# Performance work log

Measured on AMD Instinct MI355X. Metric: run time of the kernel, lower is better.

Reference implementation:

```python
import jax, jax.numpy as jnp
import numpy as np

HEADS = 4
OUT_DIM = 32
NUM_NODES = 10000
NUM_EDGES = 640000  # avg degree 64


def setup_inputs() -> dict:
    key = jax.random.key(0)
    k1, k2, k3, k4 = jax.random.split(key, 4)
    HE = HEADS * NUM_EDGES
    x_i = jax.random.normal(k1, (HE, OUT_DIM), dtype=jnp.float32)
    x_j = jax.random.normal(k2, (HE, OUT_DIM), dtype=jnp.float32)
    # glorot init for a: [heads, 1, 2*out_dim]
    fan = 1 + 2 * OUT_DIM
    limit = np.sqrt(6.0 / fan)
    a = jax.random.uniform(k3, (HEADS, 1, 2 * OUT_DIM), dtype=jnp.float32,
                           minval=-limit, maxval=limit)
    # edge_index[1] holds per-head-offset destination node ids in [0, heads*num_nodes)
    edge_index = jax.random.randint(k4, (2, HE), 0, HEADS * NUM_NODES, dtype=jnp.int64)
    return {"x_i": x_i, "x_j": x_j, "a": a, "edge_index": edge_index,
            "num_nodes": NUM_NODES}


def reference(x_i, x_j, a, edge_index, num_nodes):
    heads = a.shape[0]
    two_d = a.shape[2]
    E = x_i.shape[0] // heads
    # cat features, reshape to [heads, E, 2D]
    e_ = jnp.concatenate([x_i, x_j], axis=1).reshape(heads, E, two_d)
    # per-head score: mm(e_[h], a[h].T) -> [E, 1]; vectorized over heads
    scores = jnp.einsum("hed,hd->he", e_, a[:, 0, :])  # [heads, E]
    e = jax.nn.leaky_relu(scores, 0.2).reshape(heads * E, 1)
    # segment softmax over destination ids (PyG-style)
    idx = edge_index[1]
    num_seg = num_nodes * heads
    seg_max = jax.ops.segment_max(e, idx, num_segments=num_seg)  # [num_seg, 1]
    out = jnp.exp(e - seg_max[idx])
    seg_sum = jax.ops.segment_sum(out, idx, num_segments=num_seg)
    return out / (seg_sum[idx] + 1e-16)
```

## Files before the change

kernel.cpp:

```cpp
#include <hip/hip_runtime.h>


#define LRELU_SLOPE 0.2f
#define NSEG 40000
#define NPART 256
#define TPB_A 1024
#define ROWS_PER_BLK 128

__global__ __launch_bounds__(TPB_A, 1)
void score_part_kernel(const float* __restrict__ x_i,
                       const float* __restrict__ x_j,
                       const float* __restrict__ a,
                       const int* __restrict__ idx,
                       float* __restrict__ p_out,
                       float* __restrict__ partials,
                       int HE, int E, int a_len, int nchunks) {
    extern __shared__ float seg_lds[];
    __shared__ float a_sh[512];
    int t = threadIdx.x;
    if (t < a_len) a_sh[t] = a[t];
    for (int i = t; i < NSEG; i += TPB_A) seg_lds[i] = 0.0f;
    __syncthreads();

    int sub = t & 7;
    int rl  = t >> 3;

    for (int c = blockIdx.x; c < nchunks; c += NPART) {
        int r = c * ROWS_PER_BLK + rl;
        if (r < HE) {
            int h = r / E;
            const float4 xi = *(const float4*)(x_i + (size_t)r * 32 + sub * 4);
            const float4 xj = *(const float4*)(x_j + (size_t)r * 32 + sub * 4);
            const float4 a1 = *(const float4*)(a_sh + h * 64 + sub * 4);
            const float4 a2 = *(const float4*)(a_sh + h * 64 + 32 + sub * 4);

            float p = xi.x * a1.x + xi.y * a1.y + xi.z * a1.z + xi.w * a1.w
                    + xj.x * a2.x + xj.y * a2.y + xj.z * a2.z + xj.w * a2.w;
            p += __shfl_xor(p, 1);
            p += __shfl_xor(p, 2);
            p += __shfl_xor(p, 4);

            if (sub == 0) {
                float s = (p > 0.0f) ? p : LRELU_SLOPE * p;
                float pe = expf(s);
                p_out[r] = pe;
                atomicAdd(&seg_lds[idx[r]], pe);
            }
        }
    }
    __syncthreads();
    float* dst = partials + (size_t)blockIdx.x * NSEG;
    for (int i = t; i < NSEG; i += TPB_A) dst[i] = seg_lds[i];
}

__global__ void reduce_kernel(const float* __restrict__ partials,
                              float* __restrict__ seg_sum) {
    int tseg = blockIdx.x * blockDim.x + threadIdx.x;
    if (tseg >= NSEG) return;
    const float* p = partials + tseg;
    float s = 0.0f;
#pragma unroll 8
    for (int b = 0; b < NPART; ++b) s += p[(size_t)b * NSEG];
    seg_sum[tseg] = s;
}

__global__ void norm4_kernel(const int4* __restrict__ idx4,
                             const float* __restrict__ seg_sum,
                             float4* __restrict__ inout4, int n4) {
    int i = blockIdx.x * blockDim.x + threadIdx.x;
    if (i >= n4) return;
    float4 p = inout4[i];
    int4 id = idx4[i];
    p.x = p.x / (seg_sum[id.x] + 1e-16f);
    p.y = p.y / (seg_sum[id.y] + 1e-16f);
    p.z = p.z / (seg_sum[id.z] + 1e-16f);
    p.w = p.w / (seg_sum[id.w] + 1e-16f);
    inout4[i] = p;
}

__global__ void score_exp_atomic_kernel(const float* __restrict__ x_i,
                                        const float* __restrict__ x_j,
                                        const float* __restrict__ a,
                                        const int* __restrict__ idx,
                                        float* __restrict__ p_out,
                                        float* __restrict__ seg_sum,
                                        int HE, int E, int a_len) {
    __shared__ float a_sh[512];
    int t = threadIdx.x;
    if (t < a_len) a_sh[t] = a[t];
    __syncthreads();

    int lane = t & 63;
    int wave = t >> 6;
    int sub  = lane & 7;
    int rl   = lane >> 3;
    int r = blockIdx.x * 32 + wave * 8 + rl;
    if (r >= HE) return;

    int h = r / E;
    const float4 xi = *(const float4*)(x_i + (size_t)r * 32 + sub * 4);
    const float4 xj = *(const float4*)(x_j + (size_t)r * 32 + sub * 4);
    const float4 a1 = *(const float4*)(a_sh + h * 64 + sub * 4);
    const float4 a2 = *(const float4*)(a_sh + h * 64 + 32 + sub * 4);

    float p = xi.x * a1.x + xi.y * a1.y + xi.z * a1.z + xi.w * a1.w
            + xj.x * a2.x + xj.y * a2.y + xj.z * a2.z + xj.w * a2.w;
    p += __shfl_xor(p, 1);
    p += __shfl_xor(p, 2);
    p += __shfl_xor(p, 4);

    if (sub == 0) {
        float s = (p > 0.0f) ? p : LRELU_SLOPE * p;
        float pe = expf(s);
        p_out[r] = pe;
        atomicAdd(&seg_sum[idx[r]], pe);
    }
}

extern "C" void kernel_launch(void* const* d_in, const int* in_sizes, int n_in,
                              void* d_out, int out_size, void* d_ws, size_t ws_size,
                              hipStream_t stream) {
    const float* x_i = (const float*)d_in[0];
    const float* x_j = (const float*)d_in[1];
    const float* a   = (const float*)d_in[2];
    const int* edge_index = (const int*)d_in[3];
    const int num_nodes = 10000;

    const int HE    = in_sizes[0] / 32;
    const int a_len = in_sizes[2];
    const int heads = a_len / 64;
    const int E     = HE / heads;
    const int num_seg = heads * num_nodes;

    const int* idx = edge_index + HE;
    float* out = (float*)d_out;

    float* seg_sum  = (float*)d_ws;
    float* partials = (float*)d_ws + 40960;
    size_t need = (40960 + (size_t)NPART * NSEG) * sizeof(float);

    const int nchunks = (HE + ROWS_PER_BLK - 1) / ROWS_PER_BLK;

    if (num_seg == NSEG && ws_size >= need) {
        static bool attr_set = false;
        if (!attr_set) {
            (void)hipFuncSetAttribute((const void*)score_part_kernel,
                                      hipFuncAttributeMaxDynamicSharedMemorySize,
                                      NSEG * (int)sizeof(float));
            attr_set = true;
        }
        hipLaunchKernelGGL(score_part_kernel, dim3(NPART), dim3(TPB_A),
                           NSEG * sizeof(float), stream,
                           x_i, x_j, a, idx, out, partials, HE, E, a_len, nchunks);
        hipLaunchKernelGGL(reduce_kernel, dim3((NSEG + 255) / 256), dim3(256),
                           0, stream, partials, seg_sum);
    } else {
        hipMemsetAsync(seg_sum, 0, (size_t)num_seg * sizeof(float), stream);
        hipLaunchKernelGGL(score_exp_atomic_kernel, dim3((HE + 31) / 32), dim3(256),
                           0, stream, x_i, x_j, a, idx, out, seg_sum, HE, E, a_len);
    }

    hipLaunchKernelGGL(norm4_kernel, dim3((HE / 4 + 255) / 256), dim3(256),
                       0, stream, (const int4*)idx, seg_sum, (float4*)out, HE / 4);
}
```

Before: 674.3 us.

## Batch four chunks per iteration in score kernel to overlap loads

The score/partial-sum kernel now processes four row chunks per loop iteration, issuing all x_i/x_j and index loads before the compute and LDS atomics, so more memory requests are in flight per wave. The per-row integer division for the head index becomes a comparison against chunks-per-head, LDS zeroing and partial write-back use float4, and launch bounds are relaxed. The reduce unroll goes from 8 to 16, and the fast path now requires HE to be a multiple of the chunk size. Holding four groups of loads at once raises register pressure.

```diff
diff --git a/kernel.cpp b/kernel.cpp
--- a/kernel.cpp
+++ b/kernel.cpp
@@ -6,8 +6,57 @@
 #define NPART 256
 #define TPB_A 1024
 #define ROWS_PER_BLK 128
-
-__global__ __launch_bounds__(TPB_A, 1)
+#define UNROLL_A 4
+
+template<bool GUARD>
+__device__ __forceinline__ void process_group(
+    int c0, int nchunks, int rl, int sub, int heads, int cph,
+    const float* __restrict__ x_i, const float* __restrict__ x_j,
+    const int* __restrict__ idx, const float* __restrict__ a_sh,
+    float* __restrict__ p_out, float* __restrict__ seg_lds)
+{
+    float4 xi[UNROLL_A], xj[UNROLL_A];
+    int id[UNROLL_A];
+    int rr[UNROLL_A];
+    bool v[UNROLL_A];
+
+#pragma unroll
+    for (int u = 0; u < UNROLL_A; ++u) {
+        int c = c0 + u;
+        v[u] = !GUARD || (c < nchunks);
+        rr[u] = c * ROWS_PER_BLK + rl;
+        if (v[u]) {
+            xi[u] = *(const float4*)(x_i + (size_t)rr[u] * 32 + sub * 4);
+            xj[u] = *(const float4*)(x_j + (size_t)rr[u] * 32 + sub * 4);
+        }
+    }
+#pragma unroll
+    for (int u = 0; u < UNROLL_A; ++u) {
+        if (v[u] && sub == 0) id[u] = idx[rr[u]];
+    }
+#pragma unroll
+    for (int u = 0; u < UNROLL_A; ++u) {
+        if (GUARD && !v[u]) continue;
+        int c = c0 + u;
+        int h = 0;
+        for (int k = 1; k < heads; ++k) h += (c >= k * cph) ? 1 : 0;
+        const float4 a1 = *(const float4*)(a_sh + h * 64 + sub * 4);
+        const float4 a2 = *(const float4*)(a_sh + h * 64 + 32 + sub * 4);
+        float p = xi[u].x * a1.x + xi[u].y * a1.y + xi[u].z * a1.z + xi[u].w * a1.w
+                + xj[u].x * a2.x + xj[u].y * a2.y + xj[u].z * a2.z + xj[u].w * a2.w;
+        p += __shfl_xor(p, 1);
+        p += __shfl_xor(p, 2);
+        p += __shfl_xor(p, 4);
+        if (sub == 0) {
+            float s = (p > 0.0f) ? p : LRELU_SLOPE * p;
+            float pe = expf(s);
+            p_out[rr[u]] = pe;
+            atomicAdd(&seg_lds[id[u]], pe);
+        }
+    }
+}
+
+__global__ __launch_bounds__(TPB_A, 4)
 void score_part_kernel(const float* __restrict__ x_i,
                        const float* __restrict__ x_j,
                        const float* __restrict__ a,
@@ -19,38 +68,27 @@
     __shared__ float a_sh[512];
     int t = threadIdx.x;
     if (t < a_len) a_sh[t] = a[t];
-    for (int i = t; i < NSEG; i += TPB_A) seg_lds[i] = 0.0f;
+    float4* seg4 = (float4*)seg_lds;
+    for (int i = t; i < NSEG / 4; i += TPB_A) seg4[i] = make_float4(0, 0, 0, 0);
     __syncthreads();
 
-    int sub = t & 7;
-    int rl  = t >> 3;
-
-    for (int c = blockIdx.x; c < nchunks; c += NPART) {
-        int r = c * ROWS_PER_BLK + rl;
-        if (r < HE) {
-            int h = r / E;
-            const float4 xi = *(const float4*)(x_i + (size_t)r * 32 + sub * 4);
-            const float4 xj = *(const float4*)(x_j + (size_t)r * 32 + sub * 4);
-            const float4 a1 = *(const float4*)(a_sh + h * 64 + sub * 4);
-            const float4 a2 = *(const float4*)(a_sh + h * 64 + 32 + sub * 4);
-
-            float p = xi.x * a1.x + xi.y * a1.y + xi.z * a1.z + xi.w * a1.w
-                    + xj.x * a2.x + xj.y * a2.y + xj.z * a2.z + xj.w * a2.w;
-            p += __shfl_xor(p, 1);
-            p += __shfl_xor(p, 2);
-            p += __shfl_xor(p, 4);
-
-            if (sub == 0) {
-                float s = (p > 0.0f) ? p : LRELU_SLOPE * p;
-                float pe = expf(s);
-                p_out[r] = pe;
-                atomicAdd(&seg_lds[idx[r]], pe);
-            }
-        }
-    }
+    const int sub = t & 7;
+    const int rl  = t >> 3;
+    const int heads = a_len >> 6;
+    const int cph = E / ROWS_PER_BLK;
+
+    int c0 = blockIdx.x * UNROLL_A;
+    const int stride = NPART * UNROLL_A;
+    for (; c0 + UNROLL_A <= nchunks; c0 += stride)
+        process_group<false>(c0, nchunks, rl, sub, heads, cph,
+                             x_i, x_j, idx, a_sh, p_out, seg_lds);
+    if (c0 < nchunks)
+        process_group<true>(c0, nchunks, rl, sub, heads, cph,
+                            x_i, x_j, idx, a_sh, p_out, seg_lds);
+
     __syncthreads();
-    float* dst = partials + (size_t)blockIdx.x * NSEG;
-    for (int i = t; i < NSEG; i += TPB_A) dst[i] = seg_lds[i];
+    float4* dst = (float4*)(partials + (size_t)blockIdx.x * NSEG);
+    for (int i = t; i < NSEG / 4; i += TPB_A) dst[i] = seg4[i];
 }
 
 __global__ void reduce_kernel(const float* __restrict__ partials,
@@ -59,7 +97,7 @@
     if (tseg >= NSEG) return;
     const float* p = partials + tseg;
     float s = 0.0f;
-#pragma unroll 8
+#pragma unroll 16
     for (int b = 0; b < NPART; ++b) s += p[(size_t)b * NSEG];
     seg_sum[tseg] = s;
 }
@@ -141,7 +179,7 @@
 
     const int nchunks = (HE + ROWS_PER_BLK - 1) / ROWS_PER_BLK;
 
-    if (num_seg == NSEG && ws_size >= need) {
+    if (num_seg == NSEG && ws_size >= need && (HE % ROWS_PER_BLK) == 0) {
         static bool attr_set = false;
         if (!attr_set) {
             (void)hipFuncSetAttribute((const void*)score_part_kernel,
```

Measured after the change: 659.0 us. -2.3%, faster.
